# Optimization experiments

Hardware: AMD Instinct MI355X
Metric: run time of the kernel (lower is better)

Reference implementation:

```python
import jax, jax.numpy as jnp
import numpy as np

IMG = 416                      # image_shape
DIST = 1075.0                  # isocenter_distance
N_ANG = 320                    # 360 / rotation_resolution(=1.125 deg)
N_DET = IMG                    # detector bins
N_SAMP = IMG                   # integration samples per ray
SCALE = 512.0 / 416.0 * 0.03   # self.scale


def _ray_coords():
    """Pixel-space sample coordinates for every (angle, detector, sample).
    Returns cols, rows of shape [N_ANG, N_DET, N_SAMP] and the step length dt."""
    thetas = (jnp.arange(N_ANG, dtype=jnp.float32) * np.float32(2.0 * np.pi / N_ANG))
    half_diag = (IMG / 2.0) * np.sqrt(2.0)
    gamma_max = np.float32(np.arcsin(half_diag / DIST))  # half fan angle covering image
    gammas = jnp.linspace(-gamma_max, gamma_max, N_DET, dtype=jnp.float32)
    ray_len = np.float32(IMG * np.sqrt(2.0))             # chord length through image
    ts = jnp.linspace(np.float32(DIST - ray_len / 2.0),
                      np.float32(DIST + ray_len / 2.0), N_SAMP, dtype=jnp.float32)
    dt = float(ray_len / (N_SAMP - 1))

    th = thetas[:, None, None]        # [A,1,1]
    gm = gammas[None, :, None]        # [1,D,1]
    t = ts[None, None, :]             # [1,1,S]
    # source position on circle of radius DIST, ray direction toward detector
    sx = np.float32(DIST) * jnp.cos(th)
    sy = np.float32(DIST) * jnp.sin(th)
    x = sx - t * jnp.cos(th + gm)     # [A,D,S] world coords (isocenter at origin)
    y = sy - t * jnp.sin(th + gm)
    ctr = np.float32((IMG - 1) / 2.0)
    return x + ctr, y + ctr, dt       # pixel (col, row) coordinates


def _bilinear(img, cols, rows):
    """Zero-padded bilinear sampling of img[H,W] at float (row,col) coords."""
    c0 = jnp.floor(cols)
    r0 = jnp.floor(rows)
    wc = cols - c0
    wr = rows - r0
    c0i = c0.astype(jnp.int32)
    r0i = r0.astype(jnp.int32)

    def g(ri, ci):
        inb = (ri >= 0) & (ri < IMG) & (ci >= 0) & (ci < IMG)
        v = img[jnp.clip(ri, 0, IMG - 1), jnp.clip(ci, 0, IMG - 1)]
        return jnp.where(inb, v, jnp.float32(0.0))

    return (g(r0i, c0i) * (1 - wr) * (1 - wc)
            + g(r0i, c0i + 1) * (1 - wr) * wc
            + g(r0i + 1, c0i) * wr * (1 - wc)
            + g(r0i + 1, c0i + 1) * wr * wc)


def fan_beam_fp(vol):
    """vol: [B,H,W] -> sinogram [B, N_ANG, N_DET] via ray integration."""
    cols, rows, dt = _ray_coords()
    proj_one = lambda img: _bilinear(img, cols, rows).sum(axis=-1) * jnp.float32(dt)
    return jax.vmap(proj_one)(vol)


def setup_inputs() -> dict:
    key = jax.random.key(0)
    k1, k2 = jax.random.split(key)
    inp = jax.random.normal(k1, (1, 1, IMG, IMG), dtype=jnp.float32)
    tgt = jax.random.normal(k2, (1, 1, IMG, IMG), dtype=jnp.float32)
    return {"input": inp, "target": tgt}


def reference(input, target):
    input_proj = fan_beam_fp(input[:, 0])   # squeeze(1)
    target_proj = fan_beam_fp(target[:, 0])
    return jnp.mean((input_proj - target_proj) ** 2) * jnp.float32(SCALE)
```

## Files before the change

### kernel.cpp

```cpp
#include <hip/hip_runtime.h>
#include <math.h>

#define IMG 416
#define N_ANG 320
#define N_DET 416
#define N_SAMP 416

#define GSTRIDE 464
#define GROWS   432
#define GBYTES  ((size_t)GROWS * GSTRIDE)
#define GWORDS  (GROWS * GSTRIDE / 4)

#define SPLANE  (N_ANG * N_DET)
#define SBYTES  ((size_t)4 * SPLANE * sizeof(float))
#define WSNEED  (GBYTES + SBYTES)

#define LROWS   228
#define LSTRIDE 232

typedef float vfloat2 __attribute__((ext_vector_type(2)));

__global__ __launch_bounds__(256) void pack_kernel(const float* __restrict__ a,
                                                   const float* __restrict__ b,
                                                   unsigned int* __restrict__ G,
                                                   float* __restrict__ out) {
    int i = blockIdx.x * 256 + threadIdx.x;
    if (i == 0) out[0] = 0.0f;
    if (i >= GWORDS) return;
    int pr = i / (GSTRIDE / 4);
    int wc = i - pr * (GSTRIDE / 4);
    int r  = pr - 8;
    int c0 = wc * 4 - 8;
    float v[4];
    #pragma unroll
    for (int j = 0; j < 4; ++j) {
        int c = c0 + j;
        float val = 0.0f;
        if ((unsigned)r < (unsigned)IMG && (unsigned)c < (unsigned)IMG) {
            int idx = r * IMG + c;
            val = a[idx] - b[idx];
        }
        v[j] = val;
    }
    unsigned int u = __builtin_amdgcn_cvt_pk_fp8_f32(v[0], v[1], 0u, false);
    u = __builtin_amdgcn_cvt_pk_fp8_f32(v[2], v[3], u, true);
    G[i] = u;
}

__global__ void zero_out_kernel(float* __restrict__ out) {
    if (threadIdx.x == 0) out[0] = 0.0f;
}

__global__ __launch_bounds__(448) void proj_lds(const unsigned int* __restrict__ G,
                                                float* __restrict__ S,
                                                float theta_step, float gmax,
                                                float gstep, float t0,
                                                float dtstep) {
    __shared__ unsigned char L[LROWS * LSTRIDE];

    const int blk = blockIdx.x;
    const int a  = blk >> 2;
    const int q  = blk & 3;
    const int qi = q >> 1, qj = q & 1;
    const int r0 = qi ? 222 : -2;
    const int c0 = qj ? 220 : -4;
    const int nrows = qi ? 197 : 227;

    {
        const int gbase = ((r0 + 8) * GSTRIDE + (c0 + 8)) >> 2;
        const int total = nrows * 58;
        for (int i = threadIdx.x; i < total; i += 448) {
            int rr = i / 58;
            int cc = i - rr * 58;
            unsigned int w = G[gbase + rr * 116 + cc];
            *(unsigned int*)(&L[rr * LSTRIDE + cc * 4]) = w;
        }
    }
    __syncthreads();

    const int d = threadIdx.x;
    if (d < N_DET) {
        const float theta = (float)a * theta_step;
        const float gamma = fmaf((float)d, gstep, -gmax);
        float s1, c1, s2, c2;
        sincosf(theta, &s1, &c1);
        sincosf(theta + gamma, &s2, &c2);
        const float sx = fmaf(1075.0f, c1, 207.5f);
        const float sy = fmaf(1075.0f, s1, 207.5f);

        const float C0 = fmaf(-t0, c2, sx), dc = dtstep * c2;
        const float R0 = fmaf(-t0, s2, sy), dr = dtstep * s2;

        const float cl = qj ? 224.0f : -2.0f, ch = qj ? 418.0f : 224.0f;
        const float rl = qi ? 224.0f : -2.0f, rh = qi ? 418.0f : 224.0f;

        int klo = 0, khi = N_SAMP - 1;
        auto clip1 = [&](float X0, float dX, float lo, float hi) {
            if (fabsf(dX) < 1e-8f) {
                if (!(X0 >= lo && X0 < hi)) { klo = 1; khi = 0; }
            } else {
                float x1 = (X0 - hi) / dX;
                float x2 = (X0 - lo) / dX;
                x1 = fminf(fmaxf(x1, -1e6f), 1e6f);
                x2 = fminf(fmaxf(x2, -1e6f), 1e6f);
                int lo_k, hi_k;
                if (dX > 0.0f) { lo_k = (int)floorf(x1) + 1; hi_k = (int)floorf(x2); }
                else           { lo_k = (int)ceilf(x2);      hi_k = (int)ceilf(x1) - 1; }
                klo = max(klo, lo_k);
                khi = min(khi, hi_k);
            }
        };
        clip1(C0, dc, cl, ch);
        clip1(R0, dr, rl, rh);

        float acc = 0.0f;
        if (klo <= khi) {
            float colR = fmaf(-(float)klo, dc, C0) - (float)c0;
            float rowR = fmaf(-(float)klo, dr, R0) - (float)r0;
            #pragma unroll 4
            for (int k = klo; k <= khi; ++k) {
                const int ci = (int)colR;
                const int ri = (int)rowR;
                const float wc = colR - (float)ci;
                const float wr = rowR - (float)ri;
                const int base = ri * LSTRIDE + ci;
                const unsigned int b00 = L[base];
                const unsigned int b01 = L[base + 1];
                const unsigned int b10 = L[base + LSTRIDE];
                const unsigned int b11 = L[base + LSTRIDE + 1];
                const vfloat2 lo2 = __builtin_amdgcn_cvt_pk_f32_fp8(b00 | (b01 << 8), false);
                const vfloat2 hi2 = __builtin_amdgcn_cvt_pk_f32_fp8(b10 | (b11 << 8), false);
                const float top = fmaf(wc, lo2[1] - lo2[0], lo2[0]);
                const float bot = fmaf(wc, hi2[1] - hi2[0], hi2[0]);
                acc = fmaf(wr, bot - top, acc + top);
                colR -= dc;
                rowR -= dr;
            }
        }
        S[q * SPLANE + a * N_DET + d] = acc;
    }
}

__global__ __launch_bounds__(256) void reduce_kernel(const float* __restrict__ S,
                                                     float* __restrict__ out,
                                                     float coef) {
    const int i = blockIdx.x * 256 + threadIdx.x;
    float v = 0.0f;
    if (i < SPLANE)
        v = (S[i] + S[SPLANE + i]) + (S[2 * SPLANE + i] + S[3 * SPLANE + i]);
    float sq = v * v;
    #pragma unroll
    for (int m = 32; m > 0; m >>= 1) sq += __shfl_down(sq, m, 64);
    __shared__ float w[4];
    const int lane = threadIdx.x & 63;
    if (lane == 0) w[threadIdx.x >> 6] = sq;
    __syncthreads();
    if (threadIdx.x == 0)
        atomicAdd(out, (w[0] + w[1] + w[2] + w[3]) * coef);
}

__global__ __launch_bounds__(256) void proj_fused(const float* __restrict__ imgA,
                                                  const float* __restrict__ imgB,
                                                  float* __restrict__ out,
                                                  float theta_step, float gmax,
                                                  float gstep, float t0,
                                                  float dtstep, float coef) {
    const int idx = blockIdx.x * 256 + threadIdx.x;
    const int a  = idx / N_DET;
    const int dd = idx - a * N_DET;
    const float theta = (float)a * theta_step;
    const float gamma = fmaf((float)dd, gstep, -gmax);
    float s1, c1, s2, c2;
    sincosf(theta, &s1, &c1);
    sincosf(theta + gamma, &s2, &c2);
    const float sx = 1075.0f * c1 + 207.5f;
    const float sy = 1075.0f * s1 + 207.5f;
    float acc = 0.0f;
    #pragma unroll 4
    for (int s = 0; s < N_SAMP; ++s) {
        const float t   = fmaf((float)s, dtstep, t0);
        const float col = fmaf(-t, c2, sx);
        const float row = fmaf(-t, s2, sy);
        const float c0 = floorf(col);
        const float r0 = floorf(row);
        const float wc = col - c0;
        const float wr = row - r0;
        const int ci = (int)c0;
        const int ri = (int)r0;
        auto Gv = [&](int r, int c) -> float {
            if ((unsigned)r < (unsigned)IMG && (unsigned)c < (unsigned)IMG)
                return imgA[r * IMG + c] - imgB[r * IMG + c];
            return 0.0f;
        };
        const float v00 = Gv(ri, ci);
        const float v01 = Gv(ri, ci + 1);
        const float v10 = Gv(ri + 1, ci);
        const float v11 = Gv(ri + 1, ci + 1);
        const float top = fmaf(wc, v01 - v00, v00);
        const float bot = fmaf(wc, v11 - v10, v10);
        acc += fmaf(wr, bot - top, top);
    }
    float sq = acc * acc;
    #pragma unroll
    for (int o = 32; o > 0; o >>= 1) sq += __shfl_down(sq, o, 64);
    __shared__ float wsum[4];
    const int lane = threadIdx.x & 63;
    if (lane == 0) wsum[threadIdx.x >> 6] = sq;
    __syncthreads();
    if (threadIdx.x == 0)
        atomicAdd(out, (wsum[0] + wsum[1] + wsum[2] + wsum[3]) * coef);
}

extern "C" void kernel_launch(void* const* d_in, const int* in_sizes, int n_in,
                              void* d_out, int out_size, void* d_ws, size_t ws_size,
                              hipStream_t stream) {
    const float* in = (const float*)d_in[0];
    const float* tg = (const float*)d_in[1];
    float* out = (float*)d_out;

    const double half_diag = (IMG / 2.0) * sqrt(2.0);
    const double ray_len   = IMG * sqrt(2.0);
    const float  gmax      = (float)asin(half_diag / 1075.0);
    const float  gstep     = (float)(2.0 * (double)gmax / (N_DET - 1));
    const float  t0        = (float)(1075.0 - ray_len / 2.0);
    const float  dtstep    = (float)(ray_len / (N_SAMP - 1));
    const float  theta_step = (float)(2.0 * M_PI / N_ANG);
    const double dt        = ray_len / (N_SAMP - 1);
    const double SCALE     = 512.0 / 416.0 * 0.03;
    const float  coef      = (float)(dt * dt * SCALE / ((double)N_ANG * N_DET));

    if (ws_size >= WSNEED) {
        unsigned int* G = (unsigned int*)d_ws;
        float* S = (float*)((char*)d_ws + GBYTES);
        pack_kernel<<<(GWORDS + 255) / 256, 256, 0, stream>>>(in, tg, G, out);
        proj_lds<<<N_ANG * 4, 448, 0, stream>>>(G, S, theta_step, gmax, gstep,
                                                t0, dtstep);
        reduce_kernel<<<SPLANE / 256, 256, 0, stream>>>(S, out, coef);
    } else {
        zero_out_kernel<<<1, 64, 0, stream>>>(out);
        proj_fused<<<(N_ANG * N_DET) / 256, 256, 0, stream>>>(
            in, tg, out, theta_step, gmax, gstep, t0, dtstep, coef);
    }
}
```

Measured before the change: 105.1 us.

## Pack 2x2 fp8 quads per word and use 4x4 LDS tiles with atomics

The difference image is now stored as one 32-bit word per pixel that holds its 2x2 neighbourhood in fp8, so each bilinear sample needs one LDS load instead of four byte loads. The projection is split into 16 tiles per angle instead of 4, and each block's partial ray sums go into a single sinogram plane through atomicAdd, which the pack kernel zeroes. This cuts LDS traffic and the per-block working set and shrinks the reduction input. The cost is a 4x larger packed image, more blocks that each redo the ray setup, and atomic contention on the sinogram.

```diff
diff --git a/kernel.cpp b/kernel.cpp
--- a/kernel.cpp
+++ b/kernel.cpp
@@ -6,148 +6,153 @@
 #define N_DET 416
 #define N_SAMP 416
 
-#define GSTRIDE 464
-#define GROWS   432
-#define GBYTES  ((size_t)GROWS * GSTRIDE)
-#define GWORDS  (GROWS * GSTRIDE / 4)
+#define QSTRIDE 424
+#define QROWS   428
+#define QWORDS  (QROWS * QSTRIDE)
+#define QALLOC_BYTES ((size_t)(QWORDS + 32) * 4)
 
 #define SPLANE  (N_ANG * N_DET)
-#define SBYTES  ((size_t)4 * SPLANE * sizeof(float))
-#define WSNEED  (GBYTES + SBYTES)
-
-#define LROWS   228
-#define LSTRIDE 232
+#define SBYTES1 ((size_t)SPLANE * sizeof(float))
+#define WS_ATM  (QALLOC_BYTES + SBYTES1)
+
+#define TILE  105
+#define LROWS 108
+#define LSTR  116
+#define NCH   29
+#define LDSW  (LROWS * LSTR)
 
 typedef float vfloat2 __attribute__((ext_vector_type(2)));
 
-__global__ __launch_bounds__(256) void pack_kernel(const float* __restrict__ a,
-                                                   const float* __restrict__ b,
-                                                   unsigned int* __restrict__ G,
-                                                   float* __restrict__ out) {
+__global__ __launch_bounds__(256) void pack_q(const float* __restrict__ a,
+                                              const float* __restrict__ b,
+                                              unsigned int* __restrict__ Q,
+                                              float* __restrict__ S,
+                                              float* __restrict__ out) {
     int i = blockIdx.x * 256 + threadIdx.x;
     if (i == 0) out[0] = 0.0f;
-    if (i >= GWORDS) return;
-    int pr = i / (GSTRIDE / 4);
-    int wc = i - pr * (GSTRIDE / 4);
-    int r  = pr - 8;
-    int c0 = wc * 4 - 8;
-    float v[4];
-    #pragma unroll
-    for (int j = 0; j < 4; ++j) {
-        int c = c0 + j;
-        float val = 0.0f;
-        if ((unsigned)r < (unsigned)IMG && (unsigned)c < (unsigned)IMG) {
-            int idx = r * IMG + c;
-            val = a[idx] - b[idx];
-        }
-        v[j] = val;
-    }
-    unsigned int u = __builtin_amdgcn_cvt_pk_fp8_f32(v[0], v[1], 0u, false);
-    u = __builtin_amdgcn_cvt_pk_fp8_f32(v[2], v[3], u, true);
-    G[i] = u;
+    if (i < QWORDS) {
+        int pr = i / QSTRIDE;
+        int pc = i - pr * QSTRIDE;
+        int r = pr - 4;
+        int c = pc - 4;
+        auto dv = [&](int rr, int cc) -> float {
+            bool in = ((unsigned)rr < (unsigned)IMG) & ((unsigned)cc < (unsigned)IMG);
+            int idx = in ? rr * IMG + cc : 0;
+            float v = a[idx] - b[idx];
+            return in ? v : 0.0f;
+        };
+        unsigned int u = __builtin_amdgcn_cvt_pk_fp8_f32(dv(r, c), dv(r + 1, c), 0u, false);
+        u = __builtin_amdgcn_cvt_pk_fp8_f32(dv(r, c + 1), dv(r + 1, c + 1), u, true);
+        Q[i] = u;
+    } else {
+        int j = i - QWORDS;
+        if (j < SPLANE) S[j] = 0.0f;
+    }
 }
 
 __global__ void zero_out_kernel(float* __restrict__ out) {
     if (threadIdx.x == 0) out[0] = 0.0f;
 }
 
-__global__ __launch_bounds__(448) void proj_lds(const unsigned int* __restrict__ G,
-                                                float* __restrict__ S,
-                                                float theta_step, float gmax,
-                                                float gstep, float t0,
-                                                float dtstep) {
-    __shared__ unsigned char L[LROWS * LSTRIDE];
-
-    const int blk = blockIdx.x;
-    const int a  = blk >> 2;
-    const int q  = blk & 3;
-    const int qi = q >> 1, qj = q & 1;
-    const int r0 = qi ? 222 : -2;
-    const int c0 = qj ? 220 : -4;
-    const int nrows = qi ? 197 : 227;
+__global__ __launch_bounds__(448) void proj_q(const unsigned int* __restrict__ Q,
+                                              float* __restrict__ S,
+                                              float theta_step, float gmax,
+                                              float gstep, float t0,
+                                              float dtstep) {
+    __shared__ unsigned int L[LDSW];
+
+    const int blk  = blockIdx.x;
+    const int a    = blk >> 4;
+    const int tile = blk & 15;
+    const int ty   = tile >> 2, tx = tile & 3;
+
+    const int rli = -2 + 105 * ty;
+    const int cli = -2 + 105 * tx;
+
+    const int c4v  = cli + 2;
+    const int c0w  = c4v & ~3;
+    const int coff = c4v - c0w;
+    const int qrow0 = rli + 2;
 
     {
-        const int gbase = ((r0 + 8) * GSTRIDE + (c0 + 8)) >> 2;
-        const int total = nrows * 58;
-        for (int i = threadIdx.x; i < total; i += 448) {
-            int rr = i / 58;
-            int cc = i - rr * 58;
-            unsigned int w = G[gbase + rr * 116 + cc];
-            *(unsigned int*)(&L[rr * LSTRIDE + cc * 4]) = w;
+        const uint4* Q4 = (const uint4*)Q;
+        const int gbase4 = qrow0 * (QSTRIDE / 4) + (c0w >> 2);
+        for (int s = threadIdx.x; s < LROWS * NCH; s += 448) {
+            int rr = s / NCH;
+            int k  = s - rr * NCH;
+            uint4 w = Q4[gbase4 + rr * (QSTRIDE / 4) + k];
+            *(uint4*)(&L[rr * LSTR + 4 * k]) = w;
         }
     }
     __syncthreads();
 
     const int d = threadIdx.x;
-    if (d < N_DET) {
-        const float theta = (float)a * theta_step;
-        const float gamma = fmaf((float)d, gstep, -gmax);
-        float s1, c1, s2, c2;
-        sincosf(theta, &s1, &c1);
-        sincosf(theta + gamma, &s2, &c2);
-        const float sx = fmaf(1075.0f, c1, 207.5f);
-        const float sy = fmaf(1075.0f, s1, 207.5f);
-
-        const float C0 = fmaf(-t0, c2, sx), dc = dtstep * c2;
-        const float R0 = fmaf(-t0, s2, sy), dr = dtstep * s2;
-
-        const float cl = qj ? 224.0f : -2.0f, ch = qj ? 418.0f : 224.0f;
-        const float rl = qi ? 224.0f : -2.0f, rh = qi ? 418.0f : 224.0f;
-
-        int klo = 0, khi = N_SAMP - 1;
-        auto clip1 = [&](float X0, float dX, float lo, float hi) {
-            if (fabsf(dX) < 1e-8f) {
-                if (!(X0 >= lo && X0 < hi)) { klo = 1; khi = 0; }
-            } else {
-                float x1 = (X0 - hi) / dX;
-                float x2 = (X0 - lo) / dX;
-                x1 = fminf(fmaxf(x1, -1e6f), 1e6f);
-                x2 = fminf(fmaxf(x2, -1e6f), 1e6f);
-                int lo_k, hi_k;
-                if (dX > 0.0f) { lo_k = (int)floorf(x1) + 1; hi_k = (int)floorf(x2); }
-                else           { lo_k = (int)ceilf(x2);      hi_k = (int)ceilf(x1) - 1; }
-                klo = max(klo, lo_k);
-                khi = min(khi, hi_k);
-            }
-        };
-        clip1(C0, dc, cl, ch);
-        clip1(R0, dr, rl, rh);
-
+    if (d >= N_DET) return;
+
+    const float theta = (float)a * theta_step;
+    const float gamma = fmaf((float)d, gstep, -gmax);
+    float s1, c1, s2, c2;
+    sincosf(theta, &s1, &c1);
+    sincosf(theta + gamma, &s2, &c2);
+    const float sx = fmaf(1075.0f, c1, 207.5f);
+    const float sy = fmaf(1075.0f, s1, 207.5f);
+
+    const float C0 = fmaf(-t0, c2, sx), dc = dtstep * c2;
+    const float R0 = fmaf(-t0, s2, sy), dr = dtstep * s2;
+
+    const float cl = (float)cli, ch = (float)(cli + 105);
+    const float rl = (float)rli, rh = (float)(rli + 105);
+
+    int klo = 0, khi = N_SAMP - 1;
+    auto clip1 = [&](float X0, float dX, float lo, float hi) {
+        if (fabsf(dX) < 1e-8f) {
+            if (!(X0 >= lo && X0 < hi)) { klo = 1; khi = 0; }
+        } else {
+            float x1 = (X0 - hi) / dX;
+            float x2 = (X0 - lo) / dX;
+            x1 = fminf(fmaxf(x1, -1e6f), 1e6f);
+            x2 = fminf(fmaxf(x2, -1e6f), 1e6f);
+            int lo_k, hi_k;
+            if (dX > 0.0f) { lo_k = (int)floorf(x1) + 1; hi_k = (int)floorf(x2); }
+            else           { lo_k = (int)ceilf(x2);      hi_k = (int)ceilf(x1) - 1; }
+            klo = max(klo, lo_k);
+            khi = min(khi, hi_k);
+        }
+    };
+    clip1(C0, dc, cl, ch);
+    clip1(R0, dr, rl, rh);
+
+    if (klo <= khi) {
+        const float cbias = (float)(cli - coff - 2);
+        const float rbias = (float)(rli - 2);
+        float colR = fmaf(-(float)klo, dc, C0) - cbias;
+        float rowR = fmaf(-(float)klo, dr, R0) - rbias;
         float acc = 0.0f;
-        if (klo <= khi) {
-            float colR = fmaf(-(float)klo, dc, C0) - (float)c0;
-            float rowR = fmaf(-(float)klo, dr, R0) - (float)r0;
-            #pragma unroll 4
-            for (int k = klo; k <= khi; ++k) {
-                const int ci = (int)colR;
-                const int ri = (int)rowR;
-                const float wc = colR - (float)ci;
-                const float wr = rowR - (float)ri;
-                const int base = ri * LSTRIDE + ci;
-                const unsigned int b00 = L[base];
-                const unsigned int b01 = L[base + 1];
-                const unsigned int b10 = L[base + LSTRIDE];
-                const unsigned int b11 = L[base + LSTRIDE + 1];
-                const vfloat2 lo2 = __builtin_amdgcn_cvt_pk_f32_fp8(b00 | (b01 << 8), false);
-                const vfloat2 hi2 = __builtin_amdgcn_cvt_pk_f32_fp8(b10 | (b11 << 8), false);
-                const float top = fmaf(wc, lo2[1] - lo2[0], lo2[0]);
-                const float bot = fmaf(wc, hi2[1] - hi2[0], hi2[0]);
-                acc = fmaf(wr, bot - top, acc + top);
-                colR -= dc;
-                rowR -= dr;
-            }
+        #pragma unroll 4
+        for (int k = klo; k <= khi; ++k) {
+            const float cf = floorf(colR);
+            const float rf = floorf(rowR);
+            const float wc = colR - cf;
+            const float wr = rowR - rf;
+            const int widx = (int)fmaf(rf, (float)LSTR, cf);
+            const unsigned int w = L[widx];
+            const vfloat2 X = __builtin_amdgcn_cvt_pk_f32_fp8(w, false);
+            const vfloat2 Y = __builtin_amdgcn_cvt_pk_f32_fp8(w, true);
+            const float top = fmaf(wc, Y[0] - X[0], X[0]);
+            const float bot = fmaf(wc, Y[1] - X[1], X[1]);
+            acc = fmaf(wr, bot - top, acc + top);
+            colR -= dc;
+            rowR -= dr;
         }
-        S[q * SPLANE + a * N_DET + d] = acc;
-    }
-}
-
-__global__ __launch_bounds__(256) void reduce_kernel(const float* __restrict__ S,
-                                                     float* __restrict__ out,
-                                                     float coef) {
+        atomicAdd(&S[a * N_DET + d], acc);
+    }
+}
+
+__global__ __launch_bounds__(256) void reduce_q(const float* __restrict__ S,
+                                                float* __restrict__ out,
+                                                float coef) {
     const int i = blockIdx.x * 256 + threadIdx.x;
-    float v = 0.0f;
-    if (i < SPLANE)
-        v = (S[i] + S[SPLANE + i]) + (S[2 * SPLANE + i] + S[3 * SPLANE + i]);
+    float v = (i < SPLANE) ? S[i] : 0.0f;
     float sq = v * v;
     #pragma unroll
     for (int m = 32; m > 0; m >>= 1) sq += __shfl_down(sq, m, 64);
@@ -229,13 +234,14 @@
     const double SCALE     = 512.0 / 416.0 * 0.03;
     const float  coef      = (float)(dt * dt * SCALE / ((double)N_ANG * N_DET));
 
-    if (ws_size >= WSNEED) {
-        unsigned int* G = (unsigned int*)d_ws;
-        float* S = (float*)((char*)d_ws + GBYTES);
-        pack_kernel<<<(GWORDS + 255) / 256, 256, 0, stream>>>(in, tg, G, out);
-        proj_lds<<<N_ANG * 4, 448, 0, stream>>>(G, S, theta_step, gmax, gstep,
-                                                t0, dtstep);
-        reduce_kernel<<<SPLANE / 256, 256, 0, stream>>>(S, out, coef);
+    if (ws_size >= WS_ATM) {
+        unsigned int* Q = (unsigned int*)d_ws;
+        float* S = (float*)((char*)d_ws + QALLOC_BYTES);
+        const int packN = QWORDS + SPLANE;
+        pack_q<<<(packN + 255) / 256, 256, 0, stream>>>(in, tg, Q, S, out);
+        proj_q<<<N_ANG * 16, 448, 0, stream>>>(Q, S, theta_step, gmax, gstep,
+                                               t0, dtstep);
+        reduce_q<<<(SPLANE + 255) / 256, 256, 0, stream>>>(S, out, coef);
     } else {
         zero_out_kernel<<<1, 64, 0, stream>>>(out);
         proj_fused<<<(N_ANG * N_DET) / 256, 256, 0, stream>>>(
```

Result: slower. 118.4 us (+12.7%).

## Split each ray's samples across two threads and double partial-sum planes

Applied to the files above, without the earlier changes.

Each projection block now uses 832 threads, two per detector bin, and each thread integrates half of the clipped sample range. The partial sums go to eight planes instead of four, and the reduce kernel sums all eight. The aim is more parallelism and latency hiding per block for the LDS-gather loop, at the cost of doing the per-ray setup (sincos, clipping) twice, a larger workspace, and more reduce traffic. The LDS tile copy now also loads one extra row.

```diff
diff --git a/kernel.cpp b/kernel.cpp
--- a/kernel.cpp
+++ b/kernel.cpp
@@ -12,11 +12,14 @@
 #define GWORDS  (GROWS * GSTRIDE / 4)
 
 #define SPLANE  (N_ANG * N_DET)
-#define SBYTES  ((size_t)4 * SPLANE * sizeof(float))
+#define NPLANES 8
+#define SBYTES  ((size_t)NPLANES * SPLANE * sizeof(float))
 #define WSNEED  (GBYTES + SBYTES)
 
 #define LROWS   228
 #define LSTRIDE 232
+
+#define NTHR    832
 
 typedef float vfloat2 __attribute__((ext_vector_type(2)));
 
@@ -51,11 +54,11 @@
     if (threadIdx.x == 0) out[0] = 0.0f;
 }
 
-__global__ __launch_bounds__(448) void proj_lds(const unsigned int* __restrict__ G,
-                                                float* __restrict__ S,
-                                                float theta_step, float gmax,
-                                                float gstep, float t0,
-                                                float dtstep) {
+__global__ __launch_bounds__(NTHR) void proj_lds(const unsigned int* __restrict__ G,
+                                                 float* __restrict__ S,
+                                                 float theta_step, float gmax,
+                                                 float gstep, float t0,
+                                                 float dtstep) {
     __shared__ unsigned char L[LROWS * LSTRIDE];
 
     const int blk = blockIdx.x;
@@ -64,12 +67,12 @@
     const int qi = q >> 1, qj = q & 1;
     const int r0 = qi ? 222 : -2;
     const int c0 = qj ? 220 : -4;
-    const int nrows = qi ? 197 : 227;
+    const int nrows = qi ? 198 : 228;
 
     {
         const int gbase = ((r0 + 8) * GSTRIDE + (c0 + 8)) >> 2;
         const int total = nrows * 58;
-        for (int i = threadIdx.x; i < total; i += 448) {
+        for (int i = threadIdx.x; i < total; i += NTHR) {
             int rr = i / 58;
             int cc = i - rr * 58;
             unsigned int w = G[gbase + rr * 116 + cc];
@@ -78,47 +81,54 @@
     }
     __syncthreads();
 
-    const int d = threadIdx.x;
-    if (d < N_DET) {
-        const float theta = (float)a * theta_step;
-        const float gamma = fmaf((float)d, gstep, -gmax);
-        float s1, c1, s2, c2;
-        sincosf(theta, &s1, &c1);
-        sincosf(theta + gamma, &s2, &c2);
-        const float sx = fmaf(1075.0f, c1, 207.5f);
-        const float sy = fmaf(1075.0f, s1, 207.5f);
-
-        const float C0 = fmaf(-t0, c2, sx), dc = dtstep * c2;
-        const float R0 = fmaf(-t0, s2, sy), dr = dtstep * s2;
-
-        const float cl = qj ? 224.0f : -2.0f, ch = qj ? 418.0f : 224.0f;
-        const float rl = qi ? 224.0f : -2.0f, rh = qi ? 418.0f : 224.0f;
-
-        int klo = 0, khi = N_SAMP - 1;
-        auto clip1 = [&](float X0, float dX, float lo, float hi) {
-            if (fabsf(dX) < 1e-8f) {
-                if (!(X0 >= lo && X0 < hi)) { klo = 1; khi = 0; }
-            } else {
-                float x1 = (X0 - hi) / dX;
-                float x2 = (X0 - lo) / dX;
-                x1 = fminf(fmaxf(x1, -1e6f), 1e6f);
-                x2 = fminf(fmaxf(x2, -1e6f), 1e6f);
-                int lo_k, hi_k;
-                if (dX > 0.0f) { lo_k = (int)floorf(x1) + 1; hi_k = (int)floorf(x2); }
-                else           { lo_k = (int)ceilf(x2);      hi_k = (int)ceilf(x1) - 1; }
-                klo = max(klo, lo_k);
-                khi = min(khi, hi_k);
-            }
-        };
-        clip1(C0, dc, cl, ch);
-        clip1(R0, dr, rl, rh);
-
-        float acc = 0.0f;
-        if (klo <= khi) {
-            float colR = fmaf(-(float)klo, dc, C0) - (float)c0;
-            float rowR = fmaf(-(float)klo, dr, R0) - (float)r0;
-            #pragma unroll 4
-            for (int k = klo; k <= khi; ++k) {
+    const int t = threadIdx.x;
+    const int h = (t >= N_DET) ? 1 : 0;
+    const int d = t - (h ? N_DET : 0);
+
+    const float theta = (float)a * theta_step;
+    const float gamma = fmaf((float)d, gstep, -gmax);
+    float s1, c1, s2, c2;
+    sincosf(theta, &s1, &c1);
+    sincosf(theta + gamma, &s2, &c2);
+    const float sx = fmaf(1075.0f, c1, 207.5f);
+    const float sy = fmaf(1075.0f, s1, 207.5f);
+
+    const float C0 = fmaf(-t0, c2, sx), dc = dtstep * c2;
+    const float R0 = fmaf(-t0, s2, sy), dr = dtstep * s2;
+
+    const float cl = qj ? 224.0f : -2.0f, ch = qj ? 418.0f : 224.0f;
+    const float rl = qi ? 224.0f : -2.0f, rh = qi ? 418.0f : 224.0f;
+
+    int klo = 0, khi = N_SAMP - 1;
+    auto clip1 = [&](float X0, float dX, float lo, float hi) {
+        if (fabsf(dX) < 1e-8f) {
+            if (!(X0 >= lo && X0 < hi)) { klo = 1; khi = 0; }
+        } else {
+            float x1 = (X0 - hi) / dX;
+            float x2 = (X0 - lo) / dX;
+            x1 = fminf(fmaxf(x1, -1e6f), 1e6f);
+            x2 = fminf(fmaxf(x2, -1e6f), 1e6f);
+            int lo_k, hi_k;
+            if (dX > 0.0f) { lo_k = (int)floorf(x1) + 1; hi_k = (int)floorf(x2); }
+            else           { lo_k = (int)ceilf(x2);      hi_k = (int)ceilf(x1) - 1; }
+            klo = max(klo, lo_k);
+            khi = min(khi, hi_k);
+        }
+    };
+    clip1(C0, dc, cl, ch);
+    clip1(R0, dr, rl, rh);
+
+    float acc = 0.0f;
+    const int n = khi - klo + 1;
+    if (n > 0) {
+        const int h0 = (n + 1) >> 1;
+        const int ks = h ? klo + h0 : klo;
+        const int ke = h ? khi : klo + h0 - 1;
+        if (ks <= ke) {
+            float colR = fmaf(-(float)ks, dc, C0) - (float)c0;
+            float rowR = fmaf(-(float)ks, dr, R0) - (float)r0;
+            #pragma unroll 8
+            for (int k = ks; k <= ke; ++k) {
                 const int ci = (int)colR;
                 const int ri = (int)rowR;
                 const float wc = colR - (float)ci;
@@ -137,8 +147,8 @@
                 rowR -= dr;
             }
         }
-        S[q * SPLANE + a * N_DET + d] = acc;
-    }
+    }
+    S[(q * 2 + h) * SPLANE + a * N_DET + d] = acc;
 }
 
 __global__ __launch_bounds__(256) void reduce_kernel(const float* __restrict__ S,
@@ -146,8 +156,10 @@
                                                      float coef) {
     const int i = blockIdx.x * 256 + threadIdx.x;
     float v = 0.0f;
-    if (i < SPLANE)
-        v = (S[i] + S[SPLANE + i]) + (S[2 * SPLANE + i] + S[3 * SPLANE + i]);
+    if (i < SPLANE) {
+        #pragma unroll
+        for (int p = 0; p < NPLANES; ++p) v += S[p * SPLANE + i];
+    }
     float sq = v * v;
     #pragma unroll
     for (int m = 32; m > 0; m >>= 1) sq += __shfl_down(sq, m, 64);
@@ -233,8 +245,8 @@
         unsigned int* G = (unsigned int*)d_ws;
         float* S = (float*)((char*)d_ws + GBYTES);
         pack_kernel<<<(GWORDS + 255) / 256, 256, 0, stream>>>(in, tg, G, out);
-        proj_lds<<<N_ANG * 4, 448, 0, stream>>>(G, S, theta_step, gmax, gstep,
-                                                t0, dtstep);
+        proj_lds<<<N_ANG * 4, NTHR, 0, stream>>>(G, S, theta_step, gmax, gstep,
+                                                 t0, dtstep);
         reduce_kernel<<<SPLANE / 256, 256, 0, stream>>>(S, out, coef);
     } else {
         zero_out_kernel<<<1, 64, 0, stream>>>(out);
```

New measurement: 110.2 us. 4.9% more time.
